# Performance work log

Measured on AMD Instinct MI355X. Metric: run time of the kernel, lower is better.

## Reference

```python
import jax, jax.numpy as jnp
import numpy as np
import math

B, H_IM, W_IM, HDIM, HEADS, PS = 16, 56, 56, 512, 8, 7


def setup_inputs() -> dict:
    key = jax.random.key(0)
    ks = jax.random.split(key, 4)
    x = jax.random.normal(ks[0], (B, H_IM * W_IM, HDIM), jnp.float32)
    mask = jnp.zeros((1, 1, H_IM, W_IM), jnp.bool_)
    Wqkv = jax.random.normal(ks[1], (HDIM, 3 * HDIM), jnp.float32) * 0.02
    Wproj = jax.random.normal(ks[2], (HDIM, HDIM), jnp.float32) * 0.02
    bproj = jnp.zeros((HDIM,), jnp.float32)
    rel_bias = jax.random.normal(ks[3], (HEADS, PS * PS, PS * PS), jnp.float32) * 0.02
    return {"x": x, "mask": mask, "Wqkv": Wqkv, "Wproj": Wproj,
            "bproj": bproj, "rel_bias": rel_bias, "H": H_IM, "W": W_IM}


def reference(x, mask, Wqkv, Wproj, bproj, rel_bias, H, W):
    b = x.shape[0]
    ps, g, hd = PS, HEADS, HDIM
    dh = hd // g
    scale = dh ** (-0.5)

    qkv = x @ Wqkv                                   # [b, H*W, 3*hd]
    qkv = qkv.reshape(b, H, W, 3 * hd)
    pad_b = int(math.ceil(H / ps)) * ps - H
    pad_r = int(math.ceil(W / ps)) * ps - W
    qkv = jnp.pad(qkv, ((0, 0), (0, pad_b), (0, pad_r), (0, 0)))
    kmask = jnp.pad(mask, ((0, 0), (0, 0), (0, pad_b), (0, pad_r)), constant_values=True)
    Hp, Wp = H + pad_b, W + pad_r
    sh, sw = Hp // ps, Wp // ps
    K, P = ps * ps, sh * sw

    # patchify: b (sh kh) (sw kw) c -> b (kh kw) (sh sw) c
    qkv = qkv.reshape(b, sh, ps, sw, ps, 3 * hd).transpose(0, 2, 4, 1, 3, 5).reshape(b, K, P, 3 * hd)
    kmask = kmask.reshape(1, 1, sh, ps, sw, ps).transpose(0, 1, 3, 5, 2, 4).reshape(1, 1, K, P)

    qkv = qkv.reshape(b, K, P, 3, g, dh)
    q, k, v = qkv[:, :, :, 0], qkv[:, :, :, 1], qkv[:, :, :, 2]  # each [b, K, P, g, dh]

    attn = jnp.einsum('bqpgc,bkpgc->bgqkp', q, k)    # [b, g, K, K, P]
    attn = (attn + rel_bias[None, :, :, :, None]) * scale
    m = kmask[:, None]                                # [1, 1, 1, K, P]
    attn = jnp.where(m, -jnp.inf, attn)
    attn = jax.nn.softmax(attn, axis=-2)              # softmax over key positions within window
    attn = jnp.where(m, 0.0, attn)

    out = jnp.einsum('bgqkp,bkpgc->bqpgc', attn, v)
    out = out.reshape(b, K, P, hd)
    # un-patchify: b (kh kw) (sh sw) c -> b (sh kh) (sw kw) c
    out = out.reshape(b, ps, ps, sh, sw, hd).transpose(0, 3, 1, 4, 2, 5).reshape(b, Hp, Wp, hd)
    out = out[:, :H, :W, :].reshape(b, H * W, hd)
    return out @ Wproj + bproj
```

## Files before the change

### kernel.cpp

```cpp
#include <hip/hip_runtime.h>
#include <hip/hip_bf16.h>

using bf16 = __hip_bfloat16;
using bf16x8 = __attribute__((ext_vector_type(8))) short;
using f32x4  = __attribute__((ext_vector_type(4))) float;

#define B_    16
#define HIM   56
#define WIM   56
#define HD    512
#define NHEAD 8
#define DH    64
#define NTOK  (HIM*WIM)
#define M_    (B_*NTOK)
#define K49   49

__device__ __forceinline__ void gload_lds16(const void* g, void* l) {
  __builtin_amdgcn_global_load_lds(
      (__attribute__((address_space(1))) const void*)g,
      (__attribute__((address_space(3))) void*)l, 16, 0, 0);
}

__global__ __launch_bounds__(256) void cvt_x_kernel(const float* __restrict__ in,
                                                    bf16* __restrict__ out) {
  size_t i = ((size_t)blockIdx.x * 256 + threadIdx.x) * 8;
  float4 a = *(const float4*)(in + i);
  float4 b = *(const float4*)(in + i + 4);
  union { uint4 v; bf16 h[8]; } o;
  o.h[0] = __float2bfloat16(a.x); o.h[1] = __float2bfloat16(a.y);
  o.h[2] = __float2bfloat16(a.z); o.h[3] = __float2bfloat16(a.w);
  o.h[4] = __float2bfloat16(b.x); o.h[5] = __float2bfloat16(b.y);
  o.h[6] = __float2bfloat16(b.z); o.h[7] = __float2bfloat16(b.w);
  *(uint4*)(out + i) = o.v;
}

__global__ __launch_bounds__(256) void cvt_transpose_kernel(const float* __restrict__ in,
                                                            bf16* __restrict__ out,
                                                            int K, int N) {
  int idx = blockIdx.x * 256 + threadIdx.x;
  int k = idx / N, n = idx - k * N;
  out[(size_t)n * K + k] = __float2bfloat16(in[idx]);
}

template<bool OUT_BF16, bool BIAS>
__global__ __launch_bounds__(256, 3) void gemm128_kernel(
    const bf16* __restrict__ A,
    const bf16* __restrict__ Bt,
    void* __restrict__ Cp,
    const float* __restrict__ bias,
    int M, int N, int K, int NBX)
{
  __shared__ alignas(16) bf16 lds[3][2][128 * 32];
  const int tid  = threadIdx.x;
  const int lane = tid & 63, wid = tid >> 6;
  const int l15  = lane & 15, kq = lane >> 4;
  const int wm   = wid >> 1,  wn = wid & 1;
  const int cpx = gridDim.x >> 3;
  const int wg  = (blockIdx.x & 7) * cpx + (blockIdx.x >> 3);
  const int by  = wg / NBX, bx = wg - by * NBX;
  const long arow0 = (long)by * 128;
  const long bcol0 = (long)bx * 128;

  auto stage = [&](int buf, int kt) {
    const bf16* gA = A  + arow0 * K + kt * 32;
    const bf16* gB = Bt + bcol0 * K + kt * 32;
#pragma unroll
    for (int c = 0; c < 2; ++c) {
      int s   = c * 256 + tid;
      int row = s >> 2, sl = s & 3;
      int gs  = sl ^ ((row >> 1) & 3);
      gload_lds16((const char*)(gA + (long)row * K) + gs * 16,
                  (bf16*)&lds[buf][0][(c * 256 + wid * 64) * 8]);
      gload_lds16((const char*)(gB + (long)row * K) + gs * 16,
                  (bf16*)&lds[buf][1][(c * 256 + wid * 64) * 8]);
    }
  };

  f32x4 acc[4][4] = {};
  const int NT = K >> 5;
  stage(0, 0);
  stage(1, 1);
  int cur = 0;
#pragma unroll 1
  for (int t = 0; t < NT; ++t) {
    if (t + 1 < NT) asm volatile("s_waitcnt vmcnt(4)" ::: "memory");
    else            asm volatile("s_waitcnt vmcnt(0)" ::: "memory");
    __builtin_amdgcn_s_barrier();
    asm volatile("" ::: "memory");
    if (t + 2 < NT) { int nb = cur + 2; if (nb >= 3) nb -= 3; stage(nb, t + 2); }

    bf16x8 af[4], br[4];
#pragma unroll
    for (int mt = 0; mt < 4; ++mt) {
      int row  = wm * 64 + mt * 16 + l15;
      int slot = kq ^ ((row >> 1) & 3);
      af[mt] = *(const bf16x8*)&lds[cur][0][row * 32 + slot * 8];
    }
#pragma unroll
    for (int nt2 = 0; nt2 < 4; ++nt2) {
      int row  = wn * 64 + nt2 * 16 + l15;
      int slot = kq ^ ((row >> 1) & 3);
      br[nt2] = *(const bf16x8*)&lds[cur][1][row * 32 + slot * 8];
    }
    __builtin_amdgcn_s_setprio(1);
#pragma unroll
    for (int mt = 0; mt < 4; ++mt)
#pragma unroll
      for (int nt2 = 0; nt2 < 4; ++nt2)
        acc[mt][nt2] = __builtin_amdgcn_mfma_f32_16x16x32_bf16(af[mt], br[nt2], acc[mt][nt2], 0, 0, 0);
    __builtin_amdgcn_s_setprio(0);
    ++cur; if (cur >= 3) cur = 0;
  }

  const long crow0 = arow0 + wm * 64;
  const long ccol0 = bcol0 + wn * 64;
#pragma unroll
  for (int mt = 0; mt < 4; ++mt) {
#pragma unroll
    for (int nt2 = 0; nt2 < 4; ++nt2) {
      long col = ccol0 + nt2 * 16 + l15;
      float bv = BIAS ? bias[col] : 0.f;
#pragma unroll
      for (int r = 0; r < 4; ++r) {
        long row = crow0 + mt * 16 + kq * 4 + r;
        if (OUT_BF16) {
          bf16 h = __float2bfloat16(acc[mt][nt2][r]);
          __builtin_nontemporal_store(*(const unsigned short*)&h,
                                      (unsigned short*)Cp + row * N + col);
        } else {
          __builtin_nontemporal_store(acc[mt][nt2][r] + bv, (float*)Cp + row * N + col);
        }
      }
    }
  }
}

__global__ __launch_bounds__(256) void attn_win_kernel(
    const bf16* __restrict__ qkv, const float* __restrict__ rb, bf16* __restrict__ outa)
{
  __shared__ alignas(16) bf16 Qs[64 * 72];
  __shared__ alignas(16) bf16 Ks[64 * 72];
  __shared__ alignas(16) bf16 Vt[64 * 72];
  __shared__ alignas(16) bf16 Ps[64 * 72];
  const int tid = threadIdx.x, lane = tid & 63, wid = tid >> 6;
  const int p = blockIdx.x, g = blockIdx.y, b = blockIdx.z;
  const int sh = p >> 3, sw = p & 7;
  const size_t nb = (size_t)b * NTOK;
  const int c8 = (tid & 7) * 8;

#pragma unroll
  for (int it = 0; it < 2; ++it) {
    int t = (tid >> 3) + it * 32;
    uint4 vq = {0, 0, 0, 0}, vk = vq, vv = vq;
    if (t < K49) {
      int ph = t / 7, pw = t - ph * 7;
      int n = (sh * 7 + ph) * WIM + sw * 7 + pw;
      const bf16* src = qkv + (nb + n) * 1536 + g * 64 + c8;
      vq = *(const uint4*)(src);
      vk = *(const uint4*)(src + 512);
      vv = *(const uint4*)(src + 1024);
    }
    *(uint4*)&Qs[t * 72 + c8] = vq;
    *(uint4*)&Ks[t * 72 + c8] = vk;
    union { uint4 u; unsigned short s[8]; } uv; uv.u = vv;
    unsigned short* vt16 = (unsigned short*)Vt;
#pragma unroll
    for (int e = 0; e < 8; ++e) vt16[(c8 + e) * 72 + t] = uv.s[e];
  }
  __syncthreads();

  const int l15 = lane & 15, kq = lane >> 4;
  bf16x8 aq[2];
#pragma unroll
  for (int kk = 0; kk < 2; ++kk)
    aq[kk] = *(const bf16x8*)&Qs[(wid * 16 + l15) * 72 + kk * 32 + kq * 8];
  float sv[4][4];
#pragma unroll
  for (int ct = 0; ct < 4; ++ct) {
    f32x4 acc = {0.f, 0.f, 0.f, 0.f};
#pragma unroll
    for (int kk = 0; kk < 2; ++kk) {
      bf16x8 bk = *(const bf16x8*)&Ks[(ct * 16 + l15) * 72 + kk * 32 + kq * 8];
      acc = __builtin_amdgcn_mfma_f32_16x16x32_bf16(aq[kk], bk, acc, 0, 0, 0);
    }
    int kcol = ct * 16 + l15;
#pragma unroll
    for (int r = 0; r < 4; ++r) {
      int q = wid * 16 + kq * 4 + r;
      float bias = (q < K49 && kcol < K49) ? rb[((size_t)g * K49 + q) * K49 + kcol] : 0.f;
      float v = (acc[r] + bias) * 0.125f;
      sv[ct][r] = (kcol < K49) ? v : -1e30f;
    }
  }
#pragma unroll
  for (int r = 0; r < 4; ++r) {
    float m = fmaxf(fmaxf(sv[0][r], sv[1][r]), fmaxf(sv[2][r], sv[3][r]));
#pragma unroll
    for (int d = 1; d < 16; d <<= 1) m = fmaxf(m, __shfl_xor(m, d));
    float e0 = __expf(sv[0][r] - m), e1 = __expf(sv[1][r] - m);
    float e2 = __expf(sv[2][r] - m), e3 = __expf(sv[3][r] - m);
    float s = e0 + e1 + e2 + e3;
#pragma unroll
    for (int d = 1; d < 16; d <<= 1) s += __shfl_xor(s, d);
    float inv = 1.0f / s;
    int q = wid * 16 + kq * 4 + r;
    Ps[q * 72 +  0 + l15] = __float2bfloat16(e0 * inv);
    Ps[q * 72 + 16 + l15] = __float2bfloat16(e1 * inv);
    Ps[q * 72 + 32 + l15] = __float2bfloat16(e2 * inv);
    Ps[q * 72 + 48 + l15] = __float2bfloat16(e3 * inv);
  }
  __syncthreads();
  bf16x8 ap[2];
#pragma unroll
  for (int kk = 0; kk < 2; ++kk)
    ap[kk] = *(const bf16x8*)&Ps[(wid * 16 + l15) * 72 + kk * 32 + kq * 8];
#pragma unroll
  for (int ct = 0; ct < 4; ++ct) {
    f32x4 acc = {0.f, 0.f, 0.f, 0.f};
#pragma unroll
    for (int kk = 0; kk < 2; ++kk) {
      bf16x8 bv = *(const bf16x8*)&Vt[(ct * 16 + l15) * 72 + kk * 32 + kq * 8];
      acc = __builtin_amdgcn_mfma_f32_16x16x32_bf16(ap[kk], bv, acc, 0, 0, 0);
    }
#pragma unroll
    for (int r = 0; r < 4; ++r) {
      int q = wid * 16 + kq * 4 + r;
      if (q < K49) {
        int ph = q / 7, pw = q - ph * 7;
        int n = (sh * 7 + ph) * WIM + sw * 7 + pw;
        outa[(nb + n) * HD + g * 64 + ct * 16 + l15] = __float2bfloat16(acc[r]);
      }
    }
  }
}

extern "C" void kernel_launch(void* const* d_in, const int* in_sizes, int n_in,
                              void* d_out, int out_size, void* d_ws, size_t ws_size,
                              hipStream_t stream) {
  (void)in_sizes; (void)n_in; (void)out_size;
  const float* x     = (const float*)d_in[0];
  const float* wqkv  = (const float*)d_in[2];
  const float* wproj = (const float*)d_in[3];
  const float* bproj = (const float*)d_in[4];
  const float* rb    = (const float*)d_in[5];

  char* ws = (char*)d_ws;
  bf16* x_bf    = (bf16*)(ws);
  bf16* wqkv_t  = (bf16*)(ws + 51380224);
  bf16* wproj_t = (bf16*)(ws + 52953088);
  bf16* qkv     = (bf16*)(ws + 53477376);
  bf16* attno   = x_bf;
  float* out    = (float*)d_out;
  if (ws_size < 207618048) return;

  cvt_x_kernel<<<dim3(12544), 256, 0, stream>>>(x, x_bf);
  cvt_transpose_kernel<<<dim3(3072), 256, 0, stream>>>(wqkv, wqkv_t, 512, 1536);
  cvt_transpose_kernel<<<dim3(1024), 256, 0, stream>>>(wproj, wproj_t, 512, 512);
  gemm128_kernel<true, false><<<dim3(4704), 256, 0, stream>>>(
      x_bf, wqkv_t, (void*)qkv, nullptr, M_, 1536, 512, 12);
  attn_win_kernel<<<dim3(64, NHEAD, B_), 256, 0, stream>>>(qkv, rb, attno);
  gemm128_kernel<false, true><<<dim3(1568), 256, 0, stream>>>(
      attno, wproj_t, (void*)out, bproj, M_, 512, 512, 4);
}
```

Measured before the change: 250.9 us.

## Switch GEMMs to 256x256 tiles with 8 waves and 4-stage split A/B pipeline

Replaces the 128x128, 4-wave GEMM with a 256x256, 8-wave tile. It uses a 4-deep LDS ring with separately staged A and B halves and interleaves B-fragment loads with MFMA phases. The MFMA operands are swapped so each lane holds consecutive output columns, which allows vectorized 8- and 16-byte stores in the epilogue. The goal is higher arithmetic intensity per LDS load and fewer global stores, at the cost of fewer workgroups (392 for the projection), more LDS and registers, and possible tail imbalance.

Result: slower. 257.8 us (+2.7%).

```diff
diff --git a/kernel.cpp b/kernel.cpp
--- a/kernel.cpp
+++ b/kernel.cpp
@@ -43,93 +43,123 @@
 }
 
 template<bool OUT_BF16, bool BIAS>
-__global__ __launch_bounds__(256, 3) void gemm128_kernel(
+__global__ __launch_bounds__(512, 2) void gemm256_kernel(
     const bf16* __restrict__ A,
     const bf16* __restrict__ Bt,
     void* __restrict__ Cp,
     const float* __restrict__ bias,
     int M, int N, int K, int NBX)
 {
-  __shared__ alignas(16) bf16 lds[3][2][128 * 32];
+  __shared__ alignas(16) bf16 lds[2][4][256 * 32];
   const int tid  = threadIdx.x;
   const int lane = tid & 63, wid = tid >> 6;
   const int l15  = lane & 15, kq = lane >> 4;
-  const int wm   = wid >> 1,  wn = wid & 1;
+  const int wm   = wid >> 2,  wn = wid & 3;
   const int cpx = gridDim.x >> 3;
   const int wg  = (blockIdx.x & 7) * cpx + (blockIdx.x >> 3);
   const int by  = wg / NBX, bx = wg - by * NBX;
-  const long arow0 = (long)by * 128;
-  const long bcol0 = (long)bx * 128;
-
-  auto stage = [&](int buf, int kt) {
-    const bf16* gA = A  + arow0 * K + kt * 32;
-    const bf16* gB = Bt + bcol0 * K + kt * 32;
+  const long arow0 = (long)by * 256;
+  const long bcol0 = (long)bx * 256;
+
+  auto stageHalf = [&](int ab, int j) {
+    const bf16* g = (ab ? Bt + bcol0 * K : A + arow0 * K) + j * 32;
+    bf16* lbase = &lds[ab][j & 3][0];
 #pragma unroll
     for (int c = 0; c < 2; ++c) {
-      int s   = c * 256 + tid;
+      int s   = c * 512 + tid;
       int row = s >> 2, sl = s & 3;
       int gs  = sl ^ ((row >> 1) & 3);
-      gload_lds16((const char*)(gA + (long)row * K) + gs * 16,
-                  (bf16*)&lds[buf][0][(c * 256 + wid * 64) * 8]);
-      gload_lds16((const char*)(gB + (long)row * K) + gs * 16,
-                  (bf16*)&lds[buf][1][(c * 256 + wid * 64) * 8]);
+      gload_lds16((const char*)(g + (long)row * K) + gs * 16,
+                  lbase + (c * 512 + wid * 64) * 8);
     }
   };
 
-  f32x4 acc[4][4] = {};
-  const int NT = K >> 5;
-  stage(0, 0);
-  stage(1, 1);
-  int cur = 0;
+  f32x4 acc[8][4] = {};
+
+#define KSLICE(J, VM, DOSTAGE) {                                                        \
+    const int sl4 = (J) & 3;                                                            \
+    asm volatile("s_waitcnt vmcnt(" #VM ")" ::: "memory");                              \
+    __builtin_amdgcn_s_barrier();                                                       \
+    __builtin_amdgcn_sched_barrier(0);                                                  \
+    bf16x8 af[8], bf[2];                                                                \
+    _Pragma("unroll")                                                                   \
+    for (int mt = 0; mt < 8; ++mt) {                                                    \
+      int row = wm * 128 + mt * 16 + l15;                                               \
+      af[mt] = *(const bf16x8*)&lds[0][sl4][row * 32 + ((kq ^ ((row >> 1) & 3)) << 3)]; \
+    }                                                                                   \
+    _Pragma("unroll")                                                                   \
+    for (int nt = 0; nt < 2; ++nt) {                                                    \
+      int row = wn * 64 + nt * 16 + l15;                                                \
+      bf[nt] = *(const bf16x8*)&lds[1][sl4][row * 32 + ((kq ^ ((row >> 1) & 3)) << 3)]; \
+    }                                                                                   \
+    if (DOSTAGE) stageHalf(0, (J) + 3);                                                 \
+    asm volatile("s_waitcnt lgkmcnt(0)" ::: "memory");                                  \
+    __builtin_amdgcn_sched_barrier(0);                                                  \
+    __builtin_amdgcn_s_setprio(1);                                                      \
+    _Pragma("unroll")                                                                   \
+    for (int mt = 0; mt < 8; ++mt)                                                      \
+      _Pragma("unroll")                                                                 \
+      for (int nt = 0; nt < 2; ++nt)                                                    \
+        acc[mt][nt] = __builtin_amdgcn_mfma_f32_16x16x32_bf16(bf[nt], af[mt],           \
+                                                              acc[mt][nt], 0, 0, 0);    \
+    __builtin_amdgcn_s_setprio(0);                                                      \
+    __builtin_amdgcn_s_barrier();                                                       \
+    bf16x8 bg[2];                                                                       \
+    _Pragma("unroll")                                                                   \
+    for (int nt = 0; nt < 2; ++nt) {                                                    \
+      int row = wn * 64 + (nt + 2) * 16 + l15;                                          \
+      bg[nt] = *(const bf16x8*)&lds[1][sl4][row * 32 + ((kq ^ ((row >> 1) & 3)) << 3)]; \
+    }                                                                                   \
+    if (DOSTAGE) stageHalf(1, (J) + 3);                                                 \
+    asm volatile("s_waitcnt lgkmcnt(0)" ::: "memory");                                  \
+    __builtin_amdgcn_sched_barrier(0);                                                  \
+    __builtin_amdgcn_s_setprio(1);                                                      \
+    _Pragma("unroll")                                                                   \
+    for (int mt = 0; mt < 8; ++mt)                                                      \
+      _Pragma("unroll")                                                                 \
+      for (int nt = 0; nt < 2; ++nt)                                                    \
+        acc[mt][nt + 2] = __builtin_amdgcn_mfma_f32_16x16x32_bf16(bg[nt], af[mt],       \
+                                                              acc[mt][nt + 2], 0, 0, 0);\
+    __builtin_amdgcn_s_setprio(0);                                                      \
+    __builtin_amdgcn_s_barrier();                                                       \
+  }
+
+  stageHalf(0, 0); stageHalf(1, 0);
+  stageHalf(0, 1); stageHalf(1, 1);
+  stageHalf(0, 2); stageHalf(1, 2);
+
+  const int NK = K >> 5;
 #pragma unroll 1
-  for (int t = 0; t < NT; ++t) {
-    if (t + 1 < NT) asm volatile("s_waitcnt vmcnt(4)" ::: "memory");
-    else            asm volatile("s_waitcnt vmcnt(0)" ::: "memory");
-    __builtin_amdgcn_s_barrier();
-    asm volatile("" ::: "memory");
-    if (t + 2 < NT) { int nb = cur + 2; if (nb >= 3) nb -= 3; stage(nb, t + 2); }
-
-    bf16x8 af[4], br[4];
-#pragma unroll
-    for (int mt = 0; mt < 4; ++mt) {
-      int row  = wm * 64 + mt * 16 + l15;
-      int slot = kq ^ ((row >> 1) & 3);
-      af[mt] = *(const bf16x8*)&lds[cur][0][row * 32 + slot * 8];
-    }
-#pragma unroll
-    for (int nt2 = 0; nt2 < 4; ++nt2) {
-      int row  = wn * 64 + nt2 * 16 + l15;
-      int slot = kq ^ ((row >> 1) & 3);
-      br[nt2] = *(const bf16x8*)&lds[cur][1][row * 32 + slot * 8];
-    }
-    __builtin_amdgcn_s_setprio(1);
-#pragma unroll
-    for (int mt = 0; mt < 4; ++mt)
-#pragma unroll
-      for (int nt2 = 0; nt2 < 4; ++nt2)
-        acc[mt][nt2] = __builtin_amdgcn_mfma_f32_16x16x32_bf16(af[mt], br[nt2], acc[mt][nt2], 0, 0, 0);
-    __builtin_amdgcn_s_setprio(0);
-    ++cur; if (cur >= 3) cur = 0;
-  }
-
-  const long crow0 = arow0 + wm * 64;
-  const long ccol0 = bcol0 + wn * 64;
-#pragma unroll
-  for (int mt = 0; mt < 4; ++mt) {
-#pragma unroll
-    for (int nt2 = 0; nt2 < 4; ++nt2) {
-      long col = ccol0 + nt2 * 16 + l15;
-      float bv = BIAS ? bias[col] : 0.f;
-#pragma unroll
-      for (int r = 0; r < 4; ++r) {
-        long row = crow0 + mt * 16 + kq * 4 + r;
-        if (OUT_BF16) {
-          bf16 h = __float2bfloat16(acc[mt][nt2][r]);
-          __builtin_nontemporal_store(*(const unsigned short*)&h,
-                                      (unsigned short*)Cp + row * N + col);
-        } else {
-          __builtin_nontemporal_store(acc[mt][nt2][r] + bv, (float*)Cp + row * N + col);
+  for (int j = 0; j < NK - 3; ++j) KSLICE(j, 8, true);
+  KSLICE(NK - 3, 8, false);
+  KSLICE(NK - 2, 4, false);
+  KSLICE(NK - 1, 0, false);
+#undef KSLICE
+
+  const long crow0 = arow0 + wm * 128;
+  const long ccol0 = bcol0 + wn * 64 + kq * 4;
+#pragma unroll
+  for (int mt = 0; mt < 8; ++mt) {
+    long row = crow0 + mt * 16 + l15;
+#pragma unroll
+    for (int nt = 0; nt < 4; ++nt) {
+      long col = ccol0 + nt * 16;
+      if (OUT_BF16) {
+        union { unsigned long long u; unsigned short h[4]; } pk;
+#pragma unroll
+        for (int r = 0; r < 4; ++r) {
+          bf16 hh = __float2bfloat16(acc[mt][nt][r]);
+          pk.h[r] = *(unsigned short*)&hh;
         }
+        __builtin_nontemporal_store(pk.u,
+            (unsigned long long*)((bf16*)Cp + row * N + col));
+      } else {
+        f32x4 o = acc[mt][nt];
+        if (BIAS) {
+          o[0] += bias[col];     o[1] += bias[col + 1];
+          o[2] += bias[col + 2]; o[3] += bias[col + 3];
+        }
+        __builtin_nontemporal_store(o, (f32x4*)((float*)Cp + row * N + col));
       }
     }
   }
@@ -256,9 +286,9 @@
   cvt_x_kernel<<<dim3(12544), 256, 0, stream>>>(x, x_bf);
   cvt_transpose_kernel<<<dim3(3072), 256, 0, stream>>>(wqkv, wqkv_t, 512, 1536);
   cvt_transpose_kernel<<<dim3(1024), 256, 0, stream>>>(wproj, wproj_t, 512, 512);
-  gemm128_kernel<true, false><<<dim3(4704), 256, 0, stream>>>(
-      x_bf, wqkv_t, (void*)qkv, nullptr, M_, 1536, 512, 12);
+  gemm256_kernel<true, false><<<dim3(1176), 512, 0, stream>>>(
+      x_bf, wqkv_t, (void*)qkv, nullptr, M_, 1536, 512, 6);
   attn_win_kernel<<<dim3(64, NHEAD, B_), 256, 0, stream>>>(qkv, rb, attno);
-  gemm128_kernel<false, true><<<dim3(1568), 256, 0, stream>>>(
-      attno, wproj_t, (void*)out, bproj, M_, 512, 512, 4);
-}
+  gemm256_kernel<false, true><<<dim3(392), 512, 0, stream>>>(
+      attno, wproj_t, (void*)out, bproj, M_, 512, 512, 2);
+}
```
